# Optimization experiments

Measured on AMD Instinct MI355X. Metric: run time of the kernel, lower is better.

The kernel has to match this reference:

```python
import jax, jax.numpy as jnp
import numpy as np

B, N, DIM = 4, 4096, 512
H, DH, M, ITERS = 8, 64, 256, 6
KW = 33  # residual conv kernel length (along seq)


def setup_inputs() -> dict:
    key = jax.random.key(0)
    k1, k2, k3, k4 = jax.random.split(key, 4)
    return {
        "x": jax.random.normal(k1, (B, N, DIM), dtype=jnp.float32),
        "Wqkv": jax.random.normal(k2, (DIM, 3 * H * DH), dtype=jnp.float32) * 0.02,
        "Wout": jax.random.normal(k3, (H * DH, DIM), dtype=jnp.float32) * 0.02,
        "bout": jnp.zeros((DIM,), dtype=jnp.float32),
        "res_kernel": jax.random.normal(k4, (H, 1, KW, 1), dtype=jnp.float32) * 0.1,
    }


def _pinv_iter(x):
    # Moore-Penrose iterative pseudo-inverse, 6 Newton-Schulz-like steps.
    col = jnp.abs(x).sum(-1)  # ... i
    row = jnp.abs(x).sum(-2)  # ... j
    z = jnp.swapaxes(x, -1, -2) / (jnp.max(col) * jnp.max(row))
    I = jnp.eye(x.shape[-1], dtype=x.dtype)
    for _ in range(ITERS):
        xz = x @ z
        z = 0.25 * z @ (13.0 * I - xz @ (15.0 * I - xz @ (7.0 * I - xz)))
    return z


def reference(x, Wqkv, Wout, bout, res_kernel):
    b, n, _ = x.shape
    l = n // M  # landmark pooling window (n divisible by M -> no padding branch)
    scale = DH ** -0.5

    qkv = x @ Wqkv  # [b, n, 3*h*dh]
    q, k, v = jnp.split(qkv, 3, axis=-1)
    to_bhnd = lambda t: t.reshape(b, n, H, DH).transpose(0, 2, 1, 3)
    q, k, v = to_bhnd(q), to_bhnd(k), to_bhnd(v)
    q = q * scale

    # landmarks: mean over contiguous windows of size l
    q_lm = q.reshape(b, H, M, l, DH).sum(3) / l  # [b,h,m,dh]
    k_lm = k.reshape(b, H, M, l, DH).sum(3) / l

    sim1 = jnp.einsum('bhid,bhjd->bhij', q, k_lm)     # [b,h,n,m]
    sim2 = jnp.einsum('bhid,bhjd->bhij', q_lm, k_lm)  # [b,h,m,m]
    sim3 = jnp.einsum('bhid,bhjd->bhij', q_lm, k)     # [b,h,m,n]

    attn1 = jax.nn.softmax(sim1, axis=-1)
    attn2 = jax.nn.softmax(sim2, axis=-1)
    attn3 = jax.nn.softmax(sim3, axis=-1)

    attn2_inv = _pinv_iter(attn2)
    out = (attn1 @ attn2_inv) @ (attn3 @ v)  # [b,h,n,dh]

    # depthwise residual conv along the sequence axis of v
    pad = KW // 2
    conv = jax.lax.conv_general_dilated(
        v, res_kernel,
        window_strides=(1, 1),
        padding=((pad, pad), (0, 0)),
        dimension_numbers=('NCHW', 'OIHW', 'NCHW'),
        feature_group_count=H,
    )
    out = out + conv

    out = out.transpose(0, 2, 1, 3).reshape(b, n, H * DH)
    return out @ Wout + bout
```

## Files before the change

### kernel.cpp

```cpp
#include <hip/hip_runtime.h>
#include <math.h>

constexpr int BATCH = 4;
constexpr int SEQ   = 4096;
constexpr int DIMC  = 512;
constexpr int NH    = 8;
constexpr int HD    = 64;
constexpr int NLM   = 256;
constexpr int LWIN  = 16;
constexpr int KWIN  = 33;
constexpr int BH    = BATCH * NH;

typedef __attribute__((ext_vector_type(8))) short  bfrag;
typedef __attribute__((ext_vector_type(4))) float  ffrag;
typedef __attribute__((ext_vector_type(8))) unsigned short us8;
typedef __attribute__((ext_vector_type(4))) unsigned short us4;
typedef unsigned short ush;

__device__ __forceinline__ ush f2bf(float f) {
  unsigned u = __builtin_bit_cast(unsigned, f);
  return (ush)((u + 0x7FFFu + ((u >> 16) & 1u)) >> 16);
}
__device__ __forceinline__ float bf2f(ush h) {
  unsigned u = ((unsigned)h) << 16;
  return __builtin_bit_cast(float, u);
}
__device__ __forceinline__ void splitf(float f, ush& h, ush& l) {
  h = f2bf(f);
  l = f2bf(f - bf2f(h));
}
__device__ __forceinline__ void gl_lds16(const ush* g, ush* l) {
  __builtin_amdgcn_global_load_lds(
      (const __attribute__((address_space(1))) void*)g,
      (__attribute__((address_space(3))) void*)l, 16, 0, 0);
}

__global__ void split_flat(const float* __restrict__ src, ush* __restrict__ oh,
                           ush* __restrict__ ol, int n4) {
  for (int i = blockIdx.x * 256 + threadIdx.x; i < n4; i += gridDim.x * 256) {
    float4 f = ((const float4*)src)[i];
    us4 h, l;
    float fs[4] = {f.x, f.y, f.z, f.w};
#pragma unroll
    for (int j = 0; j < 4; ++j) {
      ush hh, ll;
      splitf(fs[j], hh, ll);
      h[j] = hh; l[j] = ll;
    }
    ((us4*)oh)[i] = h;
    ((us4*)ol)[i] = l;
  }
}

__global__ __launch_bounds__(256) void transpose_split_w(const float* __restrict__ in,
                                                         ush* __restrict__ oh,
                                                         ush* __restrict__ ol,
                                                         int R, int C) {
  __shared__ float T[32][33];
  const int tid = threadIdx.x;
  const int c0 = blockIdx.x * 32, r0 = blockIdx.y * 32;
#pragma unroll
  for (int u = 0; u < 4; ++u) {
    int r = (tid >> 5) * 4 + u, cl = tid & 31;
    T[r][cl] = in[(size_t)(r0 + r) * C + c0 + cl];
  }
  __syncthreads();
#pragma unroll
  for (int u = 0; u < 4; ++u) {
    int cl = (tid >> 5) * 4 + u, rl = tid & 31;
    float f = T[rl][cl];
    ush h, l; splitf(f, h, l);
    size_t o = (size_t)(c0 + cl) * R + r0 + rl;
    oh[o] = h; ol[o] = l;
  }
}

__global__ __launch_bounds__(256) void qkv_mfma(const ush* __restrict__ xh,
                                                const ush* __restrict__ xl,
                                                const ush* __restrict__ wTh,
                                                const ush* __restrict__ wTl,
                                                ush* __restrict__ q_bf,
                                                ush* __restrict__ k_bf,
                                                ush* __restrict__ v_bf,
                                                float* __restrict__ qlm,
                                                float* __restrict__ klm) {
  __shared__ ush Ash[128][40], Asl[128][40];
  __shared__ ush Bsh[128][40], Bsl[128][40];
  const int tid = threadIdx.x;
  const int w = tid >> 6, lane = tid & 63;
  const int lm = lane & 15, lq = lane >> 4;
  const int wm = w >> 1, wn = w & 1;
  const int row0 = blockIdx.x * 128, col0 = blockIdx.y * 128;
  const ffrag fz = {0.f, 0.f, 0.f, 0.f};
  ffrag acc[4][4];
#pragma unroll
  for (int i = 0; i < 4; ++i)
#pragma unroll
    for (int j = 0; j < 4; ++j) acc[i][j] = fz;

  const int sm = tid >> 1, skoff = (tid & 1) * 16;
  for (int k0 = 0; k0 < 512; k0 += 32) {
    __syncthreads();
    {
      size_t ao = (size_t)(row0 + sm) * 512 + k0 + skoff;
      *(us8*)&Ash[sm][skoff]     = *(const us8*)&xh[ao];
      *(us8*)&Ash[sm][skoff + 8] = *(const us8*)&xh[ao + 8];
      *(us8*)&Asl[sm][skoff]     = *(const us8*)&xl[ao];
      *(us8*)&Asl[sm][skoff + 8] = *(const us8*)&xl[ao + 8];
      size_t bo = (size_t)(col0 + sm) * 512 + k0 + skoff;
      *(us8*)&Bsh[sm][skoff]     = *(const us8*)&wTh[bo];
      *(us8*)&Bsh[sm][skoff + 8] = *(const us8*)&wTh[bo + 8];
      *(us8*)&Bsl[sm][skoff]     = *(const us8*)&wTl[bo];
      *(us8*)&Bsl[sm][skoff + 8] = *(const us8*)&wTl[bo + 8];
    }
    __syncthreads();
    bfrag ah[4], al[4], bh[4], bl[4];
#pragma unroll
    for (int mt = 0; mt < 4; ++mt) {
      ah[mt] = *(const bfrag*)&Ash[64 * wm + 16 * mt + lm][8 * lq];
      al[mt] = *(const bfrag*)&Asl[64 * wm + 16 * mt + lm][8 * lq];
    }
#pragma unroll
    for (int nt = 0; nt < 4; ++nt) {
      bh[nt] = *(const bfrag*)&Bsh[64 * wn + 16 * nt + lm][8 * lq];
      bl[nt] = *(const bfrag*)&Bsl[64 * wn + 16 * nt + lm][8 * lq];
    }
#pragma unroll
    for (int mt = 0; mt < 4; ++mt)
#pragma unroll
      for (int nt = 0; nt < 4; ++nt) {
        acc[mt][nt] = __builtin_amdgcn_mfma_f32_16x16x32_bf16(ah[mt], bh[nt], acc[mt][nt], 0, 0, 0);
        acc[mt][nt] = __builtin_amdgcn_mfma_f32_16x16x32_bf16(al[mt], bh[nt], acc[mt][nt], 0, 0, 0);
        acc[mt][nt] = __builtin_amdgcn_mfma_f32_16x16x32_bf16(ah[mt], bl[nt], acc[mt][nt], 0, 0, 0);
      }
  }
#pragma unroll
  for (int mt = 0; mt < 4; ++mt) {
    int rbase = row0 + 64 * wm + 16 * mt;
    int b = rbase >> 12;
    int ntok_base = rbase & 4095;
    int win = ntok_base >> 4;
#pragma unroll
    for (int nt = 0; nt < 4; ++nt) {
      int n_local = 64 * wn + 16 * nt;
      int col = col0 + n_local + lm;
      int which = col >> 9;
      int h = (col >> 6) & 7;
      int d = col & 63;
      int bh_i = b * NH + h;
      float scale = (which == 0) ? 0.125f : 1.0f;
      float vals[4];
      float s = 0.f;
#pragma unroll
      for (int r = 0; r < 4; ++r) {
        vals[r] = acc[mt][nt][r] * scale;
        s += vals[r];
      }
      ush* dst = which == 0 ? q_bf : (which == 1 ? k_bf : v_bf);
#pragma unroll
      for (int r = 0; r < 4; ++r) {
        int ntok = ntok_base + 4 * lq + r;
        dst[((size_t)bh_i * SEQ + ntok) * HD + d] = f2bf(vals[r]);
      }
      if (which < 2) {
        s += __shfl_xor(s, 16);
        s += __shfl_xor(s, 32);
        if (lq == 0) {
          float* lmdst = which == 0 ? qlm : klm;
          lmdst[((size_t)bh_i * NLM + win) * HD + d] = s * (1.0f / LWIN);
        }
      }
    }
  }
}

__global__ __launch_bounds__(256) void sim2_softmax(const float* __restrict__ qlm,
                                                    const float* __restrict__ klm,
                                                    ush* __restrict__ a2h,
                                                    ush* __restrict__ a2l) {
  int i = blockIdx.x & 255;
  int bh = blockIdx.x >> 8;
  int j = threadIdx.x;
  __shared__ float qrow[64];
  __shared__ float red[256];
  if (j < 64) qrow[j] = qlm[((size_t)bh * NLM + i) * HD + j];
  __syncthreads();
  const float* kr = klm + ((size_t)bh * NLM + j) * HD;
  float s = 0.f;
#pragma unroll
  for (int d = 0; d < 64; d += 4) {
    float4 kv = *(const float4*)&kr[d];
    s += qrow[d] * kv.x + qrow[d + 1] * kv.y + qrow[d + 2] * kv.z + qrow[d + 3] * kv.w;
  }
  red[j] = s; __syncthreads();
  for (int off = 128; off > 0; off >>= 1) {
    if (j < off) red[j] = fmaxf(red[j], red[j + off]);
    __syncthreads();
  }
  float mx = red[0]; __syncthreads();
  float e = expf(s - mx);
  red[j] = e; __syncthreads();
  for (int off = 128; off > 0; off >>= 1) {
    if (j < off) red[j] += red[j + off];
    __syncthreads();
  }
  float val = e / red[0];
  size_t o = ((size_t)bh * NLM + i) * NLM + j;
  ush h, l; splitf(val, h, l);
  a2h[o] = h; a2l[o] = l;
}

__global__ __launch_bounds__(256) void colmax(const ush* __restrict__ a2h,
                                              float* __restrict__ red) {
  int bh = blockIdx.x;
  int t = threadIdx.x;
  const size_t base = (size_t)bh * NLM * NLM;
  float cs = 0.f;
  for (int i = 0; i < NLM; ++i) cs += bf2f(a2h[base + (size_t)i * NLM + t]);
  __shared__ float r1[256];
  r1[t] = cs; __syncthreads();
  for (int off = 128; off > 0; off >>= 1) {
    if (t < off) r1[t] = fmaxf(r1[t], r1[t + off]);
    __syncthreads();
  }
  if (t == 0) red[bh] = r1[0];
}

__global__ void finalize_scale(float* __restrict__ red) {
  if (threadIdx.x == 0) {
    float m1 = -1e30f;
    for (int i = 0; i < BH; ++i) m1 = fmaxf(m1, red[i]);
    red[64] = 1.0f / m1;
  }
}

__global__ __launch_bounds__(256) void zinit_split(const ush* __restrict__ a2h,
                                                   const ush* __restrict__ a2l,
                                                   const float* __restrict__ red,
                                                   ush* __restrict__ zAh, ush* __restrict__ zAl,
                                                   ush* __restrict__ zBh, ush* __restrict__ zBl) {
  __shared__ float T[32][33];
  const int tid = threadIdx.x;
  const int bh = blockIdx.z;
  const int j0 = blockIdx.x * 32, i0 = blockIdx.y * 32;
  const float s = red[64];
  const size_t base = (size_t)bh * NLM * NLM;
#pragma unroll
  for (int u = 0; u < 4; ++u) {
    int jl = (tid >> 5) * 4 + u, il = tid & 31;
    size_t o = base + (size_t)(j0 + jl) * NLM + i0 + il;
    float a = (bf2f(a2h[o]) + bf2f(a2l[o])) * s;
    T[jl][il] = a;
    ush h, l; splitf(a, h, l);
    zBh[o] = h; zBl[o] = l;
  }
  __syncthreads();
#pragma unroll
  for (int u = 0; u < 4; ++u) {
    int il = (tid >> 5) * 4 + u, jl = tid & 31;
    float a = T[jl][il];
    ush h, l; splitf(a, h, l);
    size_t o = base + (size_t)(i0 + il) * NLM + j0 + jl;
    zAh[o] = h; zAl[o] = l;
  }
}

__device__ __forceinline__ void stage_gemm(
    ush (*S)[2][8][64][8],
    const ush* Ah, const ush* Al, const ush* Bh, const ush* Bl,
    const ush* E1h, const ush* E1l, const ush* E2h, const ush* E2l,
    ush* oAh, ush* oAl, ush* oBh, ush* oBl,
    int M, int N, int K, float alpha, float beta, float coef,
    int bx, int by, int batch, int tid) {
  const size_t abase = (size_t)batch * M * K;
  const size_t bbase = (size_t)batch * N * K;
  const size_t ebase = (size_t)batch * M * N;
  const int w = tid >> 6, lane = tid & 63;
  const int lm = lane & 15, lq = lane >> 4;
  const int wm = w >> 1, wn = w & 1;
  const int row0 = bx * 64, col0 = by * 64;
  const bool uAl = (Al != nullptr);
  const bool uBl = (Bl != nullptr);
  const ffrag fz = {0.f, 0.f, 0.f, 0.f};
  ffrag acc[2][2] = {{fz, fz}, {fz, fz}};

  const size_t arow = abase + (size_t)(row0 + lane) * K;
  const size_t brow = bbase + (size_t)(col0 + lane) * K;

  for (int k0 = 0; k0 < K; k0 += 64) {
    __syncthreads();
#pragma unroll
    for (int ci = 0; ci < 2; ++ci) {
      int c = 2 * w + ci;
      gl_lds16(&Ah[arow + k0 + 8 * c], &S[0][0][c][0][0]);
      gl_lds16(&Bh[brow + k0 + 8 * c], &S[1][0][c][0][0]);
      if (uAl) gl_lds16(&Al[arow + k0 + 8 * c], &S[0][1][c][0][0]);
      if (uBl) gl_lds16(&Bl[brow + k0 + 8 * c], &S[1][1][c][0][0]);
    }
    __syncthreads();
#pragma unroll
    for (int ks = 0; ks < 2; ++ks) {
      bfrag ah[2], al[2], bhf[2], blf[2];
#pragma unroll
      for (int mt = 0; mt < 2; ++mt) {
        ah[mt] = *(const bfrag*)&S[0][0][4 * ks + lq][32 * wm + 16 * mt + lm][0];
        if (uAl) al[mt] = *(const bfrag*)&S[0][1][4 * ks + lq][32 * wm + 16 * mt + lm][0];
      }
#pragma unroll
      for (int nt = 0; nt < 2; ++nt) {
        bhf[nt] = *(const bfrag*)&S[1][0][4 * ks + lq][32 * wn + 16 * nt + lm][0];
        if (uBl) blf[nt] = *(const bfrag*)&S[1][1][4 * ks + lq][32 * wn + 16 * nt + lm][0];
      }
#pragma unroll
      for (int mt = 0; mt < 2; ++mt)
#pragma unroll
        for (int nt = 0; nt < 2; ++nt) {
          acc[mt][nt] = __builtin_amdgcn_mfma_f32_16x16x32_bf16(ah[mt], bhf[nt], acc[mt][nt], 0, 0, 0);
          if (uAl) acc[mt][nt] = __builtin_amdgcn_mfma_f32_16x16x32_bf16(al[mt], bhf[nt], acc[mt][nt], 0, 0, 0);
          if (uBl) acc[mt][nt] = __builtin_amdgcn_mfma_f32_16x16x32_bf16(ah[mt], blf[nt], acc[mt][nt], 0, 0, 0);
        }
    }
  }
#pragma unroll
  for (int mt = 0; mt < 2; ++mt)
#pragma unroll
    for (int nt = 0; nt < 2; ++nt) {
      int n = col0 + 32 * wn + 16 * nt + lm;
#pragma unroll
      for (int r = 0; r < 4; ++r) {
        int m = row0 + 32 * wm + 16 * mt + 4 * lq + r;
        float c = acc[mt][nt][r];
        float e = 0.f;
        size_t eo = ebase + (size_t)m * N + n;
        if (E1h) {
          float t = bf2f(E1h[eo]);
          if (E1l) t += bf2f(E1l[eo]);
          e += alpha * t;
        }
        if (E2h) {
          float t = bf2f(E2h[eo]);
          if (E2l) t += bf2f(E2l[eo]);
          e += beta * t;
        }
        float y = coef * (e - c);
        ush h, l; splitf(y, h, l);
        if (oAh) {
          size_t o = ebase + (size_t)m * N + n;
          oAh[o] = h;
          if (oAl) oAl[o] = l;
        }
        if (oBh) {
          size_t o = (size_t)batch * N * M + (size_t)n * M + m;
          oBh[o] = h;
          if (oBl) oBl[o] = l;
        }
      }
    }
}

__global__ __launch_bounds__(256) void bgemm_split(
    const ush* Ah, const ush* Al, const ush* Bh, const ush* Bl,
    const ush* E1h, const ush* E1l, const ush* E2h, const ush* E2l,
    ush* oAh, ush* oAl, ush* oBh, ush* oBl,
    int M, int N, int K, float alpha, float beta, float coef) {
  __shared__ ush S[2][2][8][64][8];
  stage_gemm(S, Ah, Al, Bh, Bl, E1h, E1l, E2h, E2l, oAh, oAl, oBh, oBl,
             M, N, K, alpha, beta, coef, blockIdx.x, blockIdx.y, blockIdx.z,
             threadIdx.x);
}

__global__ __launch_bounds__(256) void ns_s2(
    const ush* Yh, const ush* Yl, const ush* zh, const ush* zl,
    ush* t2h, ush* t2l, ush* Uh, ush* Ul) {
  __shared__ ush S[2][2][8][64][8];
  const int bz = blockIdx.z, batch = bz >> 1;
  if ((bz & 1) == 0) {
    stage_gemm(S, Yh, Yl, Yh, Yl, Yh, Yl, nullptr, nullptr,
               t2h, t2l, nullptr, nullptr,
               256, 256, 256, 7.f, 0.f, 1.f,
               blockIdx.x, blockIdx.y, batch, threadIdx.x);
  } else {
    stage_gemm(S, zh, zl, Yh, Yl, nullptr, nullptr, nullptr, nullptr,
               Uh, Ul, nullptr, nullptr,
               256, 256, 256, 0.f, 0.f, -1.f,
               blockIdx.x, blockIdx.y, batch, threadIdx.x);
  }
}

__global__ __launch_bounds__(256) void vT_cvt_bf(const ush* __restrict__ v_bf,
                                                 ush* __restrict__ vT) {
  __shared__ ush T[64][72];
  const int bh = blockIdx.y;
  const int n0 = blockIdx.x * 64;
  const int tid = threadIdx.x;
  {
    int n = tid >> 2, off = (tid & 3) * 16;
    const ush* src = &v_bf[((size_t)bh * SEQ + n0 + n) * HD + off];
    *(us8*)&T[n][off] = *(const us8*)src;
    *(us8*)&T[n][off + 8] = *(const us8*)&src[8];
  }
  __syncthreads();
  {
    int d = tid >> 2, noff = (tid & 3) * 16;
    us8 o0, o1;
#pragma unroll
    for (int j = 0; j < 8; ++j) o0[j] = T[noff + j][d];
#pragma unroll
    for (int j = 0; j < 8; ++j) o1[j] = T[noff + 8 + j][d];
    ush* dst = &vT[((size_t)bh * HD + d) * SEQ + n0 + noff];
    *(us8*)dst = o0;
    *(us8*)&dst[8] = o1;
  }
}

constexpr int NCH = 4;
__global__ __launch_bounds__(256) void sim3_mfma(const float* __restrict__ qlm,
                                                 const ush* __restrict__ k_bf,
                                                 const ush* __restrict__ vT_bf,
                                                 float* __restrict__ O_part,
                                                 float* __restrict__ l_part) {
  constexpr int CHUNK = SEQ / NCH;
  __shared__ ush Qs[64][72];
  __shared__ ush Ks[128][72];
  __shared__ ush Vs[64][136];
  __shared__ ush Ps[64][136];
  const int bh = blockIdx.z;
  const int m0 = blockIdx.x * 64;
  const int n_base = blockIdx.y * CHUNK;
  const int tid = threadIdx.x;
  const int w = tid >> 6, lane = tid & 63;
  const int lm = lane & 15, lq = lane >> 4;
  {
    int m = tid >> 2, off = (tid & 3) * 16;
    const float* src = &qlm[((size_t)bh * NLM + m0 + m) * HD + off];
    us8 o0, o1;
#pragma unroll
    for (int j = 0; j < 8; ++j) o0[j] = f2bf(src[j]);
#pragma unroll
    for (int j = 0; j < 8; ++j) o1[j] = f2bf(src[8 + j]);
    *(us8*)&Qs[m][off] = o0;
    *(us8*)&Qs[m][off + 8] = o1;
  }
  const ffrag fz = {0.f, 0.f, 0.f, 0.f};
  ffrag O[4] = {fz, fz, fz, fz};
  float lsum[4] = {0.f, 0.f, 0.f, 0.f};

  for (int n0 = 0; n0 < CHUNK; n0 += 128) {
    __syncthreads();
    {
      int n = tid >> 1, off = (tid & 1) * 32;
      const ush* src = &k_bf[((size_t)bh * SEQ + n_base + n0 + n) * HD + off];
#pragma unroll
      for (int u = 0; u < 4; ++u) *(us8*)&Ks[n][off + 8 * u] = *(const us8*)&src[8 * u];
    }
    {
      int d = tid >> 2, off = (tid & 3) * 32;
      const ush* src = &vT_bf[((size_t)bh * HD + d) * SEQ + n_base + n0 + off];
#pragma unroll
      for (int u = 0; u < 4; ++u) *(us8*)&Vs[d][off + 8 * u] = *(const us8*)&src[8 * u];
    }
    __syncthreads();
    ffrag S[8] = {fz, fz, fz, fz, fz, fz, fz, fz};
#pragma unroll
    for (int ks = 0; ks < 2; ++ks) {
      bfrag a = *(const bfrag*)&Qs[16 * w + lm][32 * ks + 8 * lq];
#pragma unroll
      for (int t = 0; t < 8; ++t) {
        bfrag b = *(const bfrag*)&Ks[16 * t + lm][32 * ks + 8 * lq];
        S[t] = __builtin_amdgcn_mfma_f32_16x16x32_bf16(a, b, S[t], 0, 0, 0);
      }
    }
#pragma unroll
    for (int t = 0; t < 8; ++t)
#pragma unroll
      for (int r = 0; r < 4; ++r) {
        float p = __expf(S[t][r]);
        lsum[r] += p;
        Ps[16 * w + 4 * lq + r][16 * t + lm] = f2bf(p);
      }
    __syncthreads();
#pragma unroll
    for (int kk = 0; kk < 4; ++kk) {
      bfrag a = *(const bfrag*)&Ps[16 * w + lm][32 * kk + 8 * lq];
#pragma unroll
      for (int t2 = 0; t2 < 4; ++t2) {
        bfrag b = *(const bfrag*)&Vs[16 * t2 + lm][32 * kk + 8 * lq];
        O[t2] = __builtin_amdgcn_mfma_f32_16x16x32_bf16(a, b, O[t2], 0, 0, 0);
      }
    }
  }
#pragma unroll
  for (int r = 0; r < 4; ++r) {
#pragma unroll
    for (int off = 1; off < 16; off <<= 1) lsum[r] += __shfl_xor(lsum[r], off);
  }
  const size_t pbase = (size_t)blockIdx.y * 32 + bh;
  if (lm == 0) {
#pragma unroll
    for (int r = 0; r < 4; ++r)
      l_part[pbase * NLM + m0 + 16 * w + 4 * lq + r] = lsum[r];
  }
#pragma unroll
  for (int t2 = 0; t2 < 4; ++t2)
#pragma unroll
    for (int r = 0; r < 4; ++r) {
      int m = m0 + 16 * w + 4 * lq + r;
      int d = 16 * t2 + lm;
      O_part[(pbase * NLM + m) * HD + d] = O[t2][r];
    }
}

__global__ __launch_bounds__(256) void sim3_finalize(const float* __restrict__ O_part,
                                                     const float* __restrict__ l_part,
                                                     ush* __restrict__ svBh,
                                                     ush* __restrict__ svBl) {
  __shared__ float T[128][17];
  __shared__ float ls[128];
  const int bh = blockIdx.y;
  const int d0 = (blockIdx.x & 3) * 16;
  const int m0 = (blockIdx.x >> 2) * 128;
  const int tid = threadIdx.x;
  if (tid < 128) {
    float s = 0.f;
#pragma unroll
    for (int c = 0; c < NCH; ++c) s += l_part[(size_t)(c * 32 + bh) * NLM + m0 + tid];
    ls[tid] = s;
  }
#pragma unroll
  for (int i = 0; i < 8; ++i) {
    int e = i * 256 + tid;
    int m = e >> 4, dd = e & 15;
    float s = 0.f;
#pragma unroll
    for (int c = 0; c < NCH; ++c)
      s += O_part[(((size_t)(c * 32 + bh)) << 14) + (size_t)(m0 + m) * HD + d0 + dd];
    T[m][dd] = s;
  }
  __syncthreads();
#pragma unroll
  for (int i = 0; i < 8; ++i) {
    int e = i * 256 + tid;
    int dd = e >> 7, m = e & 127;
    float val = T[m][dd] / ls[m];
    ush h, l; splitf(val, h, l);
    size_t o = ((size_t)bh * HD + d0 + dd) * NLM + m0 + m;
    svBh[o] = h; svBl[o] = l;
  }
}

__global__ __launch_bounds__(256) void attn1_mfma(const ush* __restrict__ q_bf,
                                                  const float* __restrict__ klm,
                                                  const ush* __restrict__ ttT,
                                                  float* __restrict__ outp) {
  __shared__ ush bufA[256 * 72];
  __shared__ ush bufB[64 * 264];
  const int bh = blockIdx.y;
  const int b = bh >> 3, h = bh & 7;
  const int i0 = blockIdx.x * 64;
  const int tid = threadIdx.x;
  const int w = tid >> 6, lane = tid & 63;
  const int lm = lane & 15, lq = lane >> 4;
  {
    int m = tid >> 2, off = (tid & 3) * 16;
    const ush* src = &q_bf[((size_t)bh * SEQ + i0 + m) * HD + off];
    *(us8*)&bufB[m * 72 + off] = *(const us8*)src;
    *(us8*)&bufB[m * 72 + off + 8] = *(const us8*)&src[8];
  }
  {
    const float* kb = klm + (size_t)bh * NLM * HD;
#pragma unroll
    for (int u = 0; u < 16; ++u) {
      int e4 = u * 256 + tid;
      float4 f = ((const float4*)kb)[e4];
      int row = e4 >> 4, col = (e4 & 15) * 4;
      ush* p = &bufA[row * 72 + col];
      p[0] = f2bf(f.x); p[1] = f2bf(f.y); p[2] = f2bf(f.z); p[3] = f2bf(f.w);
    }
  }
  __syncthreads();
  const ffrag fz = {0.f, 0.f, 0.f, 0.f};
  ffrag S[16];
#pragma unroll
  for (int t = 0; t < 16; ++t) S[t] = fz;
#pragma unroll
  for (int ks = 0; ks < 2; ++ks) {
    bfrag a = *(const bfrag*)&bufB[(16 * w + lm) * 72 + 32 * ks + 8 * lq];
#pragma unroll
    for (int t = 0; t < 16; ++t) {
      bfrag bb = *(const bfrag*)&bufA[(16 * t + lm) * 72 + 32 * ks + 8 * lq];
      S[t] = __builtin_amdgcn_mfma_f32_16x16x32_bf16(a, bb, S[t], 0, 0, 0);
    }
  }
  float rinv[4];
  float ev[16][4];
#pragma unroll
  for (int r = 0; r < 4; ++r) {
    float mx = -INFINITY;
#pragma unroll
    for (int t = 0; t < 16; ++t) mx = fmaxf(mx, S[t][r]);
#pragma unroll
    for (int off = 1; off < 16; off <<= 1) mx = fmaxf(mx, __shfl_xor(mx, off));
    float sm = 0.f;
#pragma unroll
    for (int t = 0; t < 16; ++t) { ev[t][r] = __expf(S[t][r] - mx); sm += ev[t][r]; }
#pragma unroll
    for (int off = 1; off < 16; off <<= 1) sm += __shfl_xor(sm, off);
    rinv[r] = 1.0f / sm;
  }
  __syncthreads();
#pragma unroll
  for (int t = 0; t < 16; ++t)
#pragma unroll
    for (int r = 0; r < 4; ++r)
      bufB[(16 * w + 4 * lq + r) * 264 + 16 * t + lm] = f2bf(ev[t][r]);
  {
    const ush* tb = ttT + (size_t)bh * HD * NLM;
#pragma unroll
    for (int u = 0; u < 8; ++u) {
      int e8 = u * 256 + tid;
      int row = e8 >> 5, col = (e8 & 31) * 8;
      *(us8*)&bufA[row * 264 + col] = *(const us8*)&tb[row * NLM + col];
    }
  }
  __syncthreads();
  ffrag O[4] = {fz, fz, fz, fz};
#pragma unroll
  for (int kk = 0; kk < 8; ++kk) {
    bfrag a = *(const bfrag*)&bufB[(16 * w + lm) * 264 + 32 * kk + 8 * lq];
#pragma unroll
    for (int t2 = 0; t2 < 4; ++t2) {
      bfrag bb = *(const bfrag*)&bufA[(16 * t2 + lm) * 264 + 32 * kk + 8 * lq];
      O[t2] = __builtin_amdgcn_mfma_f32_16x16x32_bf16(a, bb, O[t2], 0, 0, 0);
    }
  }
#pragma unroll
  for (int t2 = 0; t2 < 4; ++t2)
#pragma unroll
    for (int r = 0; r < 4; ++r) {
      int i = i0 + 16 * w + 4 * lq + r;
      int d = 16 * t2 + lm;
      outp[((size_t)b * SEQ + i) * DIMC + h * HD + d] = O[t2][r] * rinv[r];
    }
}

__global__ __launch_bounds__(256) void conv_add_split(const float* __restrict__ outp,
                                                      const ush* __restrict__ vT,
                                                      const float* __restrict__ kern,
                                                      ush* __restrict__ oh,
                                                      ush* __restrict__ ol) {
  __shared__ float vt[64 * 97];
  __shared__ float ks[KWIN];
  const int bh = blockIdx.y;
  const int b = bh >> 3, hh = bh & 7;
  const int n0 = blockIdx.x * 64;
  const int tid = threadIdx.x;
  if (tid < KWIN) ks[tid] = kern[hh * KWIN + tid];
  for (int e = tid; e < 64 * 96; e += 256) {
    int d = e / 96, c = e % 96;
    int n = n0 - 16 + c;
    vt[d * 97 + c] = (n >= 0 && n < SEQ) ? bf2f(vT[((size_t)bh * HD + d) * SEQ + n]) : 0.f;
  }
  __syncthreads();
  const int d = tid & 63, g = tid >> 6;
  float wreg[48];
#pragma unroll
  for (int j = 0; j < 48; ++j) wreg[j] = vt[d * 97 + g * 16 + j];
#pragma unroll
  for (int nn = 0; nn < 16; ++nn) {
    float s = 0.f;
#pragma unroll
    for (int t = 0; t < KWIN; ++t) s = fmaf(ks[t], wreg[nn + t], s);
    int n = n0 + g * 16 + nn;
    size_t o = ((size_t)b * SEQ + n) * DIMC + hh * HD + d;
    float val = outp[o] + s;
    ush h, l; splitf(val, h, l);
    oh[o] = h; ol[o] = l;
  }
}

__global__ __launch_bounds__(256) void out_gemm_split(const ush* __restrict__ ah_g,
                                                      const ush* __restrict__ al_g,
                                                      const ush* __restrict__ bh_g,
                                                      const ush* __restrict__ bl_g,
                                                      const float* __restrict__ bias,
                                                      float* __restrict__ out) {
  __shared__ ush Ash[128][40], Asl[128][40];
  __shared__ ush Bsh[128][40], Bsl[128][40];
  const int tid = threadIdx.x;
  const int w = tid >> 6, lane = tid & 63;
  const int lm = lane & 15, lq = lane >> 4;
  const int wm = w >> 1, wn = w & 1;
  const int row0 = blockIdx.x * 128, col0 = blockIdx.y * 128;
  const ffrag fz = {0.f, 0.f, 0.f, 0.f};
  ffrag acc[4][4];
#pragma unroll
  for (int i = 0; i < 4; ++i)
#pragma unroll
    for (int j = 0; j < 4; ++j) acc[i][j] = fz;

  const int sm = tid >> 1, skoff = (tid & 1) * 16;
  for (int k0 = 0; k0 < 512; k0 += 32) {
    __syncthreads();
    {
      size_t ao = (size_t)(row0 + sm) * 512 + k0 + skoff;
      *(us8*)&Ash[sm][skoff]     = *(const us8*)&ah_g[ao];
      *(us8*)&Ash[sm][skoff + 8] = *(const us8*)&ah_g[ao + 8];
      *(us8*)&Asl[sm][skoff]     = *(const us8*)&al_g[ao];
      *(us8*)&Asl[sm][skoff + 8] = *(const us8*)&al_g[ao + 8];
      size_t bo = (size_t)(col0 + sm) * 512 + k0 + skoff;
      *(us8*)&Bsh[sm][skoff]     = *(const us8*)&bh_g[bo];
      *(us8*)&Bsh[sm][skoff + 8] = *(const us8*)&bh_g[bo + 8];
      *(us8*)&Bsl[sm][skoff]     = *(const us8*)&bl_g[bo];
      *(us8*)&Bsl[sm][skoff + 8] = *(const us8*)&bl_g[bo + 8];
    }
    __syncthreads();
    bfrag ah[4], al[4], bh[4], bl[4];
#pragma unroll
    for (int mt = 0; mt < 4; ++mt) {
      ah[mt] = *(const bfrag*)&Ash[64 * wm + 16 * mt + lm][8 * lq];
      al[mt] = *(const bfrag*)&Asl[64 * wm + 16 * mt + lm][8 * lq];
    }
#pragma unroll
    for (int nt = 0; nt < 4; ++nt) {
      bh[nt] = *(const bfrag*)&Bsh[64 * wn + 16 * nt + lm][8 * lq];
      bl[nt] = *(const bfrag*)&Bsl[64 * wn + 16 * nt + lm][8 * lq];
    }
#pragma unroll
    for (int mt = 0; mt < 4; ++mt)
#pragma unroll
      for (int nt = 0; nt < 4; ++nt) {
        acc[mt][nt] = __builtin_amdgcn_mfma_f32_16x16x32_bf16(ah[mt], bh[nt], acc[mt][nt], 0, 0, 0);
        acc[mt][nt] = __builtin_amdgcn_mfma_f32_16x16x32_bf16(al[mt], bh[nt], acc[mt][nt], 0, 0, 0);
        acc[mt][nt] = __builtin_amdgcn_mfma_f32_16x16x32_bf16(ah[mt], bl[nt], acc[mt][nt], 0, 0, 0);
      }
  }
#pragma unroll
  for (int mt = 0; mt < 4; ++mt)
#pragma unroll
    for (int nt = 0; nt < 4; ++nt) {
      int n = col0 + 64 * wn + 16 * nt + lm;
      float bv = bias[n];
#pragma unroll
      for (int r = 0; r < 4; ++r) {
        int m = row0 + 64 * wm + 16 * mt + 4 * lq + r;
        out[(size_t)m * 512 + n] = acc[mt][nt][r] + bv;
      }
    }
}

extern "C" void kernel_launch(void* const* d_in, const int* in_sizes, int n_in,
                              void* d_out, int out_size, void* d_ws, size_t ws_size,
                              hipStream_t stream) {
  const float* x    = (const float*)d_in[0];
  const float* Wqkv = (const float*)d_in[1];
  const float* Wout = (const float*)d_in[2];
  const float* bout = (const float*)d_in[3];
  const float* rker = (const float*)d_in[4];
  float* out = (float*)d_out;
  float* ws = (float*)d_ws;

  ush*   v_bf   = (ush*)(ws);
  ush*   q_bf   = (ush*)(ws + 4194304);
  float* regA   = ws + 8388608;
  float* regB   = ws + 16777216;
  float* qlm    = ws + 25165824;
  float* klm    = ws + 25690112;
  float* regC   = ws + 26214400;
  float* a2reg  = ws + 28311552;
  float* zAreg  = ws + 30408704;
  float* zBreg  = ws + 34603008;
  float* xzreg  = ws + 38797312;
  float* t3reg  = ws + 43515904;
  float* wqkvT  = ws + 45613056;
  float* woutT  = ws + 46399488;
  float* red    = ws + 46661632;

  ush* k_bf  = (ush*)regA;
  float* outp = regA;
  ush* xh = (ush*)regB;
  ush* xl = (ush*)(regB + 4194304);
  ush* outph = (ush*)regB;
  ush* outpl = (ush*)(regB + 4194304);
  ush* a2h = (ush*)a2reg;
  ush* a2l = (ush*)(a2reg + 1048576);
  ush* zA_[4] = {(ush*)zAreg, (ush*)(zAreg + 1048576), (ush*)(zAreg + 2097152), (ush*)(zAreg + 3145728)};
  ush* zB_[4] = {(ush*)zBreg, (ush*)(zBreg + 1048576), (ush*)(zBreg + 2097152), (ush*)(zBreg + 3145728)};
  ush* Y_h  = (ush*)xzreg;
  ush* Y_l  = (ush*)(xzreg + 1048576);
  ush* t2_h = (ush*)regC;
  ush* t2_l = (ush*)(regC + 1048576);
  ush* U_h  = (ush*)t3reg;
  ush* U_l  = (ush*)(t3reg + 1048576);
  ush* vT_bf = (ush*)zBreg;
  float* O_part = xzreg;
  float* l_part = xzreg + 2097152;
  ush* svB_h = (ush*)t3reg;
  ush* svB_l = (ush*)(t3reg + 262144);
  ush* ttT   = (ush*)regC;
  ush* wqkvT_h = (ush*)wqkvT;
  ush* wqkvT_l = (ush*)(wqkvT + 393216);
  ush* woutT_h = (ush*)woutT;
  ush* woutT_l = (ush*)(woutT + 131072);

  split_flat<<<2048, 256, 0, stream>>>(x, xh, xl, 2097152);
  transpose_split_w<<<dim3(48, 16), 256, 0, stream>>>(Wqkv, wqkvT_h, wqkvT_l, 512, 1536);
  transpose_split_w<<<dim3(16, 16), 256, 0, stream>>>(Wout, woutT_h, woutT_l, 512, 512);

  qkv_mfma<<<dim3(128, 12), 256, 0, stream>>>(xh, xl, wqkvT_h, wqkvT_l,
                                              q_bf, k_bf, v_bf, qlm, klm);

  sim2_softmax<<<8192, 256, 0, stream>>>(qlm, klm, a2h, a2l);
  colmax<<<32, 256, 0, stream>>>(a2h, red);
  finalize_scale<<<1, 64, 0, stream>>>(red);
  zinit_split<<<dim3(8, 8, 32), 256, 0, stream>>>(a2h, a2l, red,
                                                  zA_[0], zA_[1], zA_[2], zA_[3]);

  ush** zc = zA_;
  ush** zn = zB_;
  for (int it = 0; it < 6; ++it) {
    const bool zin_s  = (it == 5);
    const bool a2_s   = (it >= 4);
    const bool mid_s  = (it >= 4);
    const bool zout_s = (it >= 4);
    bgemm_split<<<dim3(4, 4, 32), 256, 0, stream>>>(
        a2h, a2_s ? a2l : nullptr,
        zc[2], zin_s ? zc[3] : nullptr,
        nullptr, nullptr, nullptr, nullptr,
        Y_h, mid_s ? Y_l : nullptr, nullptr, nullptr,
        256, 256, 256, 0.f, 0.f, -1.f);
    ns_s2<<<dim3(4, 4, 64), 256, 0, stream>>>(
        Y_h, mid_s ? Y_l : nullptr,
        zc[0], zin_s ? zc[1] : nullptr,
        t2_h, mid_s ? t2_l : nullptr,
        U_h, mid_s ? U_l : nullptr);
    bgemm_split<<<dim3(4, 4, 32), 256, 0, stream>>>(
        U_h, mid_s ? U_l : nullptr,
        t2_h, mid_s ? t2_l : nullptr,
        zc[0], zin_s ? zc[1] : nullptr,
        U_h, mid_s ? U_l : nullptr,
        zn[0], zout_s ? zn[1] : nullptr,
        zn[2], zout_s ? zn[3] : nullptr,
        256, 256, 256, -13.f, 15.f, -0.25f);
    ush** tp = zc; zc = zn; zn = tp;
  }

  vT_cvt_bf<<<dim3(64, 32), 256, 0, stream>>>(v_bf, vT_bf);
  sim3_mfma<<<dim3(4, NCH, 32), 256, 0, stream>>>(qlm, k_bf, vT_bf, O_part, l_part);
  sim3_finalize<<<dim3(8, 32), 256, 0, stream>>>(O_part, l_part, svB_h, svB_l);

  bgemm_split<<<dim3(4, 1, 32), 256, 0, stream>>>(
      zc[0], zc[1], svB_h, svB_l,
      nullptr, nullptr, nullptr, nullptr,
      nullptr, nullptr, ttT, nullptr, 256, 64, 256, 0.f, 0.f, -1.f);

  attn1_mfma<<<dim3(64, 32), 256, 0, stream>>>(q_bf, klm, ttT, outp);
  conv_add_split<<<dim3(64, 32), 256, 0, stream>>>(outp, vT_bf, rker, outph, outpl);
  out_gemm_split<<<dim3(128, 4), 256, 0, stream>>>(outph, outpl, woutT_h, woutT_l, bout, out);
}
```

Measured before the change: 739.8 us.

## Fuse pseudo-inverse iterations into persistent kernel, write V transposed, drop W low part

The 18 per-iteration Newton-Schulz launches are replaced by one persistent kernel of 512 blocks. Each group of 16 blocks handles one batch-head and synchronizes through a software global barrier built on atomics, which removes launch gaps but relies on all 512 blocks being resident at once. The QKV GEMM now writes V directly in transposed layout, so the separate transpose kernel goes away. It also drops the low-order bf16 part of the weights, cutting one MFMA per tile and the matching loads at some cost in precision. The barrier counters are zeroed in finalize_scale.

After: 1.905 ms. 157% more time.

```diff
diff --git a/kernel.cpp b/kernel.cpp
--- a/kernel.cpp
+++ b/kernel.cpp
@@ -78,14 +78,13 @@
 __global__ __launch_bounds__(256) void qkv_mfma(const ush* __restrict__ xh,
                                                 const ush* __restrict__ xl,
                                                 const ush* __restrict__ wTh,
-                                                const ush* __restrict__ wTl,
                                                 ush* __restrict__ q_bf,
                                                 ush* __restrict__ k_bf,
-                                                ush* __restrict__ v_bf,
+                                                ush* __restrict__ vT,
                                                 float* __restrict__ qlm,
                                                 float* __restrict__ klm) {
   __shared__ ush Ash[128][40], Asl[128][40];
-  __shared__ ush Bsh[128][40], Bsl[128][40];
+  __shared__ ush Bsh[128][40];
   const int tid = threadIdx.x;
   const int w = tid >> 6, lane = tid & 63;
   const int lm = lane & 15, lq = lane >> 4;
@@ -110,28 +109,23 @@
       size_t bo = (size_t)(col0 + sm) * 512 + k0 + skoff;
       *(us8*)&Bsh[sm][skoff]     = *(const us8*)&wTh[bo];
       *(us8*)&Bsh[sm][skoff + 8] = *(const us8*)&wTh[bo + 8];
-      *(us8*)&Bsl[sm][skoff]     = *(const us8*)&wTl[bo];
-      *(us8*)&Bsl[sm][skoff + 8] = *(const us8*)&wTl[bo + 8];
-    }
-    __syncthreads();
-    bfrag ah[4], al[4], bh[4], bl[4];
+    }
+    __syncthreads();
+    bfrag ah[4], al[4], bh[4];
 #pragma unroll
     for (int mt = 0; mt < 4; ++mt) {
       ah[mt] = *(const bfrag*)&Ash[64 * wm + 16 * mt + lm][8 * lq];
       al[mt] = *(const bfrag*)&Asl[64 * wm + 16 * mt + lm][8 * lq];
     }
 #pragma unroll
-    for (int nt = 0; nt < 4; ++nt) {
+    for (int nt = 0; nt < 4; ++nt)
       bh[nt] = *(const bfrag*)&Bsh[64 * wn + 16 * nt + lm][8 * lq];
-      bl[nt] = *(const bfrag*)&Bsl[64 * wn + 16 * nt + lm][8 * lq];
-    }
 #pragma unroll
     for (int mt = 0; mt < 4; ++mt)
 #pragma unroll
       for (int nt = 0; nt < 4; ++nt) {
         acc[mt][nt] = __builtin_amdgcn_mfma_f32_16x16x32_bf16(ah[mt], bh[nt], acc[mt][nt], 0, 0, 0);
         acc[mt][nt] = __builtin_amdgcn_mfma_f32_16x16x32_bf16(al[mt], bh[nt], acc[mt][nt], 0, 0, 0);
-        acc[mt][nt] = __builtin_amdgcn_mfma_f32_16x16x32_bf16(ah[mt], bl[nt], acc[mt][nt], 0, 0, 0);
       }
   }
 #pragma unroll
@@ -156,13 +150,17 @@
         vals[r] = acc[mt][nt][r] * scale;
         s += vals[r];
       }
-      ush* dst = which == 0 ? q_bf : (which == 1 ? k_bf : v_bf);
-#pragma unroll
-      for (int r = 0; r < 4; ++r) {
-        int ntok = ntok_base + 4 * lq + r;
-        dst[((size_t)bh_i * SEQ + ntok) * HD + d] = f2bf(vals[r]);
-      }
-      if (which < 2) {
+      if (which == 2) {
+        ush* dst = &vT[((size_t)bh_i * HD + d) * SEQ + ntok_base + 4 * lq];
+#pragma unroll
+        for (int r = 0; r < 4; ++r) dst[r] = f2bf(vals[r]);
+      } else {
+        ush* dst = which == 0 ? q_bf : k_bf;
+#pragma unroll
+        for (int r = 0; r < 4; ++r) {
+          int ntok = ntok_base + 4 * lq + r;
+          dst[((size_t)bh_i * SEQ + ntok) * HD + d] = f2bf(vals[r]);
+        }
         s += __shfl_xor(s, 16);
         s += __shfl_xor(s, 32);
         if (lq == 0) {
@@ -226,8 +224,10 @@
   if (t == 0) red[bh] = r1[0];
 }
 
-__global__ void finalize_scale(float* __restrict__ red) {
-  if (threadIdx.x == 0) {
+__global__ void finalize_scale(float* __restrict__ red, unsigned* __restrict__ bar) {
+  int t = threadIdx.x;
+  for (int i = t; i < 2048; i += 64) bar[i] = 0u;
+  if (t == 0) {
     float m1 = -1e30f;
     for (int i = 0; i < BH; ++i) m1 = fmaxf(m1, red[i]);
     red[64] = 1.0f / m1;
@@ -369,47 +369,71 @@
              threadIdx.x);
 }
 
-__global__ __launch_bounds__(256) void ns_s2(
-    const ush* Yh, const ush* Yl, const ush* zh, const ush* zl,
-    ush* t2h, ush* t2l, ush* Uh, ush* Ul) {
+__device__ __forceinline__ void gbar16(unsigned* cnt, unsigned* gen) {
+  __syncthreads();
+  if (threadIdx.x == 0) {
+    unsigned g = __hip_atomic_load(gen, __ATOMIC_RELAXED, __HIP_MEMORY_SCOPE_SYSTEM);
+    __threadfence_system();
+    unsigned old = __hip_atomic_fetch_add(cnt, 1u, __ATOMIC_ACQ_REL, __HIP_MEMORY_SCOPE_SYSTEM);
+    if (old == 15u) {
+      __hip_atomic_store(cnt, 0u, __ATOMIC_RELAXED, __HIP_MEMORY_SCOPE_SYSTEM);
+      __hip_atomic_fetch_add(gen, 1u, __ATOMIC_ACQ_REL, __HIP_MEMORY_SCOPE_SYSTEM);
+    } else {
+      while (__hip_atomic_load(gen, __ATOMIC_ACQUIRE, __HIP_MEMORY_SCOPE_SYSTEM) == g)
+        __builtin_amdgcn_s_sleep(2);
+    }
+    __threadfence_system();
+  }
+  __syncthreads();
+}
+
+__global__ __launch_bounds__(256, 2) void pinv_fused(
+    const ush* a2h, const ush* a2l,
+    ush* zA0, ush* zA1, ush* zA2, ush* zA3,
+    ush* zB0, ush* zB1, ush* zB2, ush* zB3,
+    ush* Y_h, ush* Y_l, ush* t2_h, ush* t2_l, ush* U_h, ush* U_l,
+    unsigned* bar) {
   __shared__ ush S[2][2][8][64][8];
-  const int bz = blockIdx.z, batch = bz >> 1;
-  if ((bz & 1) == 0) {
-    stage_gemm(S, Yh, Yl, Yh, Yl, Yh, Yl, nullptr, nullptr,
-               t2h, t2l, nullptr, nullptr,
-               256, 256, 256, 7.f, 0.f, 1.f,
-               blockIdx.x, blockIdx.y, batch, threadIdx.x);
-  } else {
-    stage_gemm(S, zh, zl, Yh, Yl, nullptr, nullptr, nullptr, nullptr,
-               Uh, Ul, nullptr, nullptr,
-               256, 256, 256, 0.f, 0.f, -1.f,
-               blockIdx.x, blockIdx.y, batch, threadIdx.x);
-  }
-}
-
-__global__ __launch_bounds__(256) void vT_cvt_bf(const ush* __restrict__ v_bf,
-                                                 ush* __restrict__ vT) {
-  __shared__ ush T[64][72];
-  const int bh = blockIdx.y;
-  const int n0 = blockIdx.x * 64;
   const int tid = threadIdx.x;
-  {
-    int n = tid >> 2, off = (tid & 3) * 16;
-    const ush* src = &v_bf[((size_t)bh * SEQ + n0 + n) * HD + off];
-    *(us8*)&T[n][off] = *(const us8*)src;
-    *(us8*)&T[n][off + 8] = *(const us8*)&src[8];
-  }
-  __syncthreads();
-  {
-    int d = tid >> 2, noff = (tid & 3) * 16;
-    us8 o0, o1;
-#pragma unroll
-    for (int j = 0; j < 8; ++j) o0[j] = T[noff + j][d];
-#pragma unroll
-    for (int j = 0; j < 8; ++j) o1[j] = T[noff + 8 + j][d];
-    ush* dst = &vT[((size_t)bh * HD + d) * SEQ + n0 + noff];
-    *(us8*)dst = o0;
-    *(us8*)&dst[8] = o1;
+  const int b = blockIdx.x;
+  const int bx = b & 3, by = (b >> 2) & 3, bz = b >> 4;
+  unsigned* cnt = bar + bz * 64;
+  unsigned* gen = cnt + 32;
+
+  ush* zc0 = zA0; ush* zc1 = zA1; ush* zc2 = zA2; ush* zc3 = zA3;
+  ush* zn0 = zB0; ush* zn1 = zB1; ush* zn2 = zB2; ush* zn3 = zB3;
+
+#pragma unroll 1
+  for (int it = 0; it < 6; ++it) {
+    const bool zin_s  = (it == 5);
+    const bool a2_s   = (it >= 4);
+    const bool mid_s  = (it >= 4);
+    const bool zout_s = (it >= 4);
+    stage_gemm(S, a2h, a2_s ? a2l : nullptr, zc2, zin_s ? zc3 : nullptr,
+               nullptr, nullptr, nullptr, nullptr,
+               Y_h, mid_s ? Y_l : nullptr, nullptr, nullptr,
+               256, 256, 256, 0.f, 0.f, -1.f, bx, by, bz, tid);
+    gbar16(cnt, gen);
+    stage_gemm(S, Y_h, mid_s ? Y_l : nullptr, Y_h, mid_s ? Y_l : nullptr,
+               Y_h, mid_s ? Y_l : nullptr, nullptr, nullptr,
+               t2_h, mid_s ? t2_l : nullptr, nullptr, nullptr,
+               256, 256, 256, 7.f, 0.f, 1.f, bx, by, bz, tid);
+    stage_gemm(S, zc0, zin_s ? zc1 : nullptr, Y_h, mid_s ? Y_l : nullptr,
+               nullptr, nullptr, nullptr, nullptr,
+               U_h, mid_s ? U_l : nullptr, nullptr, nullptr,
+               256, 256, 256, 0.f, 0.f, -1.f, bx, by, bz, tid);
+    gbar16(cnt, gen);
+    stage_gemm(S, U_h, mid_s ? U_l : nullptr, t2_h, mid_s ? t2_l : nullptr,
+               zc0, zin_s ? zc1 : nullptr,
+               U_h, mid_s ? U_l : nullptr,
+               zn0, zout_s ? zn1 : nullptr, zn2, zout_s ? zn3 : nullptr,
+               256, 256, 256, -13.f, 15.f, -0.25f, bx, by, bz, tid);
+    if (it < 5) gbar16(cnt, gen);
+    ush* t;
+    t = zc0; zc0 = zn0; zn0 = t;
+    t = zc1; zc1 = zn1; zn1 = t;
+    t = zc2; zc2 = zn2; zn2 = t;
+    t = zc3; zc3 = zn3; zn3 = t;
   }
 }
 
@@ -759,7 +783,7 @@
   float* out = (float*)d_out;
   float* ws = (float*)d_ws;
 
-  ush*   v_bf   = (ush*)(ws);
+  ush*   vT     = (ush*)(ws);
   ush*   q_bf   = (ush*)(ws + 4194304);
   float* regA   = ws + 8388608;
   float* regB   = ws + 16777216;
@@ -787,11 +811,11 @@
   ush* zB_[4] = {(ush*)zBreg, (ush*)(zBreg + 1048576), (ush*)(zBreg + 2097152), (ush*)(zBreg + 3145728)};
   ush* Y_h  = (ush*)xzreg;
   ush* Y_l  = (ush*)(xzreg + 1048576);
+  unsigned* bar = (unsigned*)(xzreg + 2097152);
   ush* t2_h = (ush*)regC;
   ush* t2_l = (ush*)(regC + 1048576);
   ush* U_h  = (ush*)t3reg;
   ush* U_l  = (ush*)(t3reg + 1048576);
-  ush* vT_bf = (ush*)zBreg;
   float* O_part = xzreg;
   float* l_part = xzreg + 2097152;
   ush* svB_h = (ush*)t3reg;
@@ -806,54 +830,30 @@
   transpose_split_w<<<dim3(48, 16), 256, 0, stream>>>(Wqkv, wqkvT_h, wqkvT_l, 512, 1536);
   transpose_split_w<<<dim3(16, 16), 256, 0, stream>>>(Wout, woutT_h, woutT_l, 512, 512);
 
-  qkv_mfma<<<dim3(128, 12), 256, 0, stream>>>(xh, xl, wqkvT_h, wqkvT_l,
-                                              q_bf, k_bf, v_bf, qlm, klm);
+  qkv_mfma<<<dim3(128, 12), 256, 0, stream>>>(xh, xl, wqkvT_h,
+                                              q_bf, k_bf, vT, qlm, klm);
 
   sim2_softmax<<<8192, 256, 0, stream>>>(qlm, klm, a2h, a2l);
   colmax<<<32, 256, 0, stream>>>(a2h, red);
-  finalize_scale<<<1, 64, 0, stream>>>(red);
+  finalize_scale<<<1, 64, 0, stream>>>(red, bar);
   zinit_split<<<dim3(8, 8, 32), 256, 0, stream>>>(a2h, a2l, red,
                                                   zA_[0], zA_[1], zA_[2], zA_[3]);
 
-  ush** zc = zA_;
-  ush** zn = zB_;
-  for (int it = 0; it < 6; ++it) {
-    const bool zin_s  = (it == 5);
-    const bool a2_s   = (it >= 4);
-    const bool mid_s  = (it >= 4);
-    const bool zout_s = (it >= 4);
-    bgemm_split<<<dim3(4, 4, 32), 256, 0, stream>>>(
-        a2h, a2_s ? a2l : nullptr,
-        zc[2], zin_s ? zc[3] : nullptr,
-        nullptr, nullptr, nullptr, nullptr,
-        Y_h, mid_s ? Y_l : nullptr, nullptr, nullptr,
-        256, 256, 256, 0.f, 0.f, -1.f);
-    ns_s2<<<dim3(4, 4, 64), 256, 0, stream>>>(
-        Y_h, mid_s ? Y_l : nullptr,
-        zc[0], zin_s ? zc[1] : nullptr,
-        t2_h, mid_s ? t2_l : nullptr,
-        U_h, mid_s ? U_l : nullptr);
-    bgemm_split<<<dim3(4, 4, 32), 256, 0, stream>>>(
-        U_h, mid_s ? U_l : nullptr,
-        t2_h, mid_s ? t2_l : nullptr,
-        zc[0], zin_s ? zc[1] : nullptr,
-        U_h, mid_s ? U_l : nullptr,
-        zn[0], zout_s ? zn[1] : nullptr,
-        zn[2], zout_s ? zn[3] : nullptr,
-        256, 256, 256, -13.f, 15.f, -0.25f);
-    ush** tp = zc; zc = zn; zn = tp;
-  }
-
-  vT_cvt_bf<<<dim3(64, 32), 256, 0, stream>>>(v_bf, vT_bf);
-  sim3_mfma<<<dim3(4, NCH, 32), 256, 0, stream>>>(qlm, k_bf, vT_bf, O_part, l_part);
+  pinv_fused<<<512, 256, 0, stream>>>(
+      a2h, a2l,
+      zA_[0], zA_[1], zA_[2], zA_[3],
+      zB_[0], zB_[1], zB_[2], zB_[3],
+      Y_h, Y_l, t2_h, t2_l, U_h, U_l, bar);
+
+  sim3_mfma<<<dim3(4, NCH, 32), 256, 0, stream>>>(qlm, k_bf, vT, O_part, l_part);
   sim3_finalize<<<dim3(8, 32), 256, 0, stream>>>(O_part, l_part, svB_h, svB_l);
 
   bgemm_split<<<dim3(4, 1, 32), 256, 0, stream>>>(
-      zc[0], zc[1], svB_h, svB_l,
+      zA_[0], zA_[1], svB_h, svB_l,
       nullptr, nullptr, nullptr, nullptr,
       nullptr, nullptr, ttT, nullptr, 256, 64, 256, 0.f, 0.f, -1.f);
 
   attn1_mfma<<<dim3(64, 32), 256, 0, stream>>>(q_bf, klm, ttT, outp);
-  conv_add_split<<<dim3(64, 32), 256, 0, stream>>>(outp, vT_bf, rker, outph, outpl);
+  conv_add_split<<<dim3(64, 32), 256, 0, stream>>>(outp, vT, rker, outph, outpl);
   out_gemm_split<<<dim3(128, 4), 256, 0, stream>>>(outph, outpl, woutT_h, woutT_l, bout, out);
 }
```
